# Performance work log

Hardware: AMD Instinct MI355X
Metric: run time of the kernel (lower is better)

## Reference

```python
import jax, jax.numpy as jnp
import numpy as np

N_BLADES = 8  # Cl(3,0): 1, e1, e2, e3 and their products (bitmask blade indexing)


def _blade_sign(a: int, b: int) -> int:
    # Sign from reordering basis vectors when multiplying blades a*b (Euclidean metric).
    a >>= 1
    s = 0
    while a:
        s += bin(a & b).count('1')
        a >>= 1
    return -1 if (s & 1) else 1


def make_cayley() -> np.ndarray:
    C = np.zeros((N_BLADES, N_BLADES, N_BLADES), dtype=np.float32)
    for a in range(N_BLADES):
        for b in range(N_BLADES):
            C[a, b, a ^ b] = float(_blade_sign(a, b))
    return C


def setup_inputs() -> dict:
    key = jax.random.key(0)
    k1, k2 = jax.random.split(key)
    B, Cin, Cout = 8192, 256, 256
    scale = 1.0 / np.sqrt(Cin * N_BLADES)
    x = jax.random.normal(k1, (B, Cin, N_BLADES), dtype=jnp.float32)
    weight = jax.random.normal(k2, (Cout, Cin, N_BLADES), dtype=jnp.float32) * scale
    bias = jnp.zeros((Cout, N_BLADES), dtype=jnp.float32)
    cayley = jnp.asarray(make_cayley())
    return {"x": x, "weight": weight, "bias": bias, "cayley": cayley}


def reference(x, weight, bias, cayley):
    # A[b,o,j,k] = sum_i W[o,i,j] * X[b,i,k]  (weight blade j times input blade k)
    A = jnp.einsum('oij,bik->bojk', weight, x)
    # Contract blade pair (j,k) into output blade l via sparse Cayley table.
    out = jnp.einsum('jkl,bojk->bol', cayley, A)
    return out + bias[None, :, :]
```

## Files before the change

kernel.cpp:

```cpp
#include <hip/hip_runtime.h>
#include <stdint.h>
#include <stddef.h>


typedef __bf16 bf16x8 __attribute__((ext_vector_type(8)));
typedef float  f32x4  __attribute__((ext_vector_type(4)));

#define BM 128
#define BN 128
#define BK 32

__device__ __forceinline__ void async_copy16(void* lds_dst, const void* g_src) {
    __builtin_amdgcn_global_load_lds(
        (__attribute__((address_space(1))) void*)g_src,
        (__attribute__((address_space(3))) void*)lds_dst,
        16, 0, 0);
}

__global__ __launch_bounds__(256) void cast_bf16_kernel(
    const float* __restrict__ in, __bf16* __restrict__ out, long n)
{
    long i = ((long)blockIdx.x * 256 + threadIdx.x) * 8;
    if (i + 8 <= n) {
        const f32x4* p = (const f32x4*)(in + i);
        f32x4 v0 = p[0];
        f32x4 v1 = p[1];
        bf16x8 o;
        o[0] = (__bf16)v0[0]; o[1] = (__bf16)v0[1];
        o[2] = (__bf16)v0[2]; o[3] = (__bf16)v0[3];
        o[4] = (__bf16)v1[0]; o[5] = (__bf16)v1[1];
        o[6] = (__bf16)v1[2]; o[7] = (__bf16)v1[3];
        *(bf16x8*)(out + i) = o;
    }
}

__global__ __launch_bounds__(256) void build_wt_kernel(
    const float* __restrict__ W,
    const float* __restrict__ cayley,
    __bf16* __restrict__ Wt,
    int Cin, int Cout)
{
    __shared__ float Cay[512];
    for (int t = threadIdx.x; t < 512; t += 256) Cay[t] = cayley[t];
    __syncthreads();

    int flat = blockIdx.x * 256 + threadIdx.x;
    int total = Cout * 8 * Cin;
    if (flat >= total) return;
    int i = flat % Cin;
    int n = flat / Cin;
    int o = n >> 3, l = n & 7;

    const float* wrow = W + ((size_t)o * Cin + i) * 8;
    float w8[8];
    #pragma unroll
    for (int j = 0; j < 8; ++j) w8[j] = wrow[j];

    bf16x8 outv;
    #pragma unroll
    for (int k = 0; k < 8; ++k) {
        float s = 0.f;
        #pragma unroll
        for (int j = 0; j < 8; ++j) s += Cay[j * 64 + k * 8 + l] * w8[j];
        outv[k] = (__bf16)s;
    }
    *(bf16x8*)(Wt + (size_t)n * (Cin * 8) + i * 8) = outv;
}

__global__ __launch_bounds__(256) void gemm_bt_kernel(
    const __bf16* __restrict__ A,
    const __bf16* __restrict__ Bt,
    const float*  __restrict__ bias,
    float* __restrict__ C,
    int M, int N, int K)
{
    __shared__ __align__(16) __bf16 As0[BM * BK];
    __shared__ __align__(16) __bf16 As1[BM * BK];
    __shared__ __align__(16) __bf16 Bs0[BN * BK];
    __shared__ __align__(16) __bf16 Bs1[BN * BK];

    const int tid  = threadIdx.x;
    const int wave = tid >> 6;
    const int lane = tid & 63;
    const int quad = lane >> 4;
    const int l16  = lane & 15;

    const int bid   = blockIdx.x;
    const int band  = (bid & 7) | ((bid >> 7) << 3);
    const int ncol  = (bid >> 3) & 15;
    const int mBase = band * BM;
    const int nBase = ncol * BN;

    const int srow = lane >> 2;
    const int sgrp = (lane & 3) ^ ((srow >> 1) & 3);

    const __bf16* gA0 = A  + (size_t)(mBase + (2 * wave + 0) * 16 + srow) * K + sgrp * 8;
    const __bf16* gA1 = A  + (size_t)(mBase + (2 * wave + 1) * 16 + srow) * K + sgrp * 8;
    const __bf16* gB0 = Bt + (size_t)(nBase + (2 * wave + 0) * 16 + srow) * K + sgrp * 8;
    const __bf16* gB1 = Bt + (size_t)(nBase + (2 * wave + 1) * 16 + srow) * K + sgrp * 8;
    const int cOff0 = (2 * wave + 0) * 512;
    const int cOff1 = (2 * wave + 1) * 512;

    const int wm = (wave >> 1) * 64;
    const int wn = (wave & 1) * 64;
    const int offq = (quad ^ ((l16 >> 1) & 3)) * 8;
    const int rowA = (wm + l16) * BK;
    const int rowB = (wn + l16) * BK;

    f32x4 acc[4][4] = {};

#define PREFETCH(BUFA, BUFB, KOFF)                       \
    do {                                                 \
        async_copy16(&BUFA[cOff0], gA0 + (KOFF));        \
        async_copy16(&BUFA[cOff1], gA1 + (KOFF));        \
        async_copy16(&BUFB[cOff0], gB0 + (KOFF));        \
        async_copy16(&BUFB[cOff1], gB1 + (KOFF));        \
    } while (0)

#define COMPUTE(BUFA, BUFB)                                               \
    do {                                                                  \
        const __bf16* fA = &BUFA[rowA] + offq;                            \
        const __bf16* fB = &BUFB[rowB] + offq;                            \
        bf16x8 af[4], bfr[4];                                             \
        _Pragma("unroll")                                                 \
        for (int mt = 0; mt < 4; ++mt)                                    \
            af[mt] = *(const bf16x8*)(fA + mt * 16 * BK);                 \
        _Pragma("unroll")                                                 \
        for (int nt = 0; nt < 4; ++nt)                                    \
            bfr[nt] = *(const bf16x8*)(fB + nt * 16 * BK);                \
        _Pragma("unroll")                                                 \
        for (int mt = 0; mt < 4; ++mt)                                    \
            _Pragma("unroll")                                             \
            for (int nt = 0; nt < 4; ++nt)                                \
                acc[mt][nt] = __builtin_amdgcn_mfma_f32_16x16x32_bf16(    \
                    af[mt], bfr[nt], acc[mt][nt], 0, 0, 0);               \
    } while (0)

    PREFETCH(As0, Bs0, 0);

    int k0 = 0;
    for (; k0 < K - 2 * BK; k0 += 2 * BK) {
        __syncthreads();
        PREFETCH(As1, Bs1, k0 + BK);
        COMPUTE(As0, Bs0);

        __syncthreads();
        PREFETCH(As0, Bs0, k0 + 2 * BK);
        COMPUTE(As1, Bs1);
    }

    __syncthreads();
    PREFETCH(As1, Bs1, k0 + BK);
    COMPUTE(As0, Bs0);

    __syncthreads();
    COMPUTE(As1, Bs1);

#undef PREFETCH
#undef COMPUTE

    float bv[4];
    #pragma unroll
    for (int nt = 0; nt < 4; ++nt)
        bv[nt] = bias[nBase + wn + nt * 16 + l16];

    #pragma unroll
    for (int mt = 0; mt < 4; ++mt) {
        #pragma unroll
        for (int nt = 0; nt < 4; ++nt) {
            const int col = nBase + wn + nt * 16 + l16;
            #pragma unroll
            for (int r = 0; r < 4; ++r) {
                const int row = mBase + wm + mt * 16 + quad * 4 + r;
                C[(size_t)row * N + col] = acc[mt][nt][r] + bv[nt];
            }
        }
    }
}

extern "C" void kernel_launch(void* const* d_in, const int* in_sizes, int n_in,
                              void* d_out, int out_size, void* d_ws, size_t ws_size,
                              hipStream_t stream) {
    const float* x      = (const float*)d_in[0];
    const float* weight = (const float*)d_in[1];
    const float* bias   = (const float*)d_in[2];
    const float* cayley = (const float*)d_in[3];
    float* out = (float*)d_out;

    const int Cout = in_sizes[2] / 8;
    const int Cin  = in_sizes[1] / (Cout * 8);
    const int Bm   = in_sizes[0] / (Cin * 8);
    const int M = Bm;
    const int N = Cout * 8;
    const int K = Cin * 8;

    __bf16* Xb = (__bf16*)d_ws;
    __bf16* Wt = (__bf16*)((char*)d_ws + (size_t)M * K * 2);

    long nx = (long)M * K;
    int castBlocks = (int)(nx / 8 / 256);
    cast_bf16_kernel<<<castBlocks, 256, 0, stream>>>(x, Xb, nx);

    int totalWt = N * Cin;
    build_wt_kernel<<<(totalWt + 255) / 256, 256, 0, stream>>>(weight, cayley, Wt, Cin, Cout);

    int grid = (M / BM) * (N / BN);
    gemm_bt_kernel<<<grid, 256, 0, stream>>>(Xb, Wt, bias, out, M, N, K);
}
```

Baseline: 199.5 us.

## Switch GEMM to 32x32x16 MFMA tiles and merge prep kernels into one launch

The GEMM inner loop moves from sixteen 16x16x32 bf16 MFMAs per wave per K-step to eight 32x32x16 MFMAs over 2x2 accumulator tiles. This cuts the number of LDS fragment loads per MFMA and uses the larger matrix instruction. The epilogue is rewritten to match the 32x32 output layout. Separately, the bf16 cast of x and the Cayley weight fold are merged into a single launch to save one kernel launch, at the cost of branch divergence by block index.

```diff
diff --git a/kernel.cpp b/kernel.cpp
--- a/kernel.cpp
+++ b/kernel.cpp
@@ -3,8 +3,9 @@
 #include <stddef.h>
 
 
-typedef __bf16 bf16x8 __attribute__((ext_vector_type(8)));
-typedef float  f32x4  __attribute__((ext_vector_type(4)));
+typedef __bf16 bf16x8  __attribute__((ext_vector_type(8)));
+typedef float  f32x4   __attribute__((ext_vector_type(4)));
+typedef float  f32x16  __attribute__((ext_vector_type(16)));
 
 #define BM 128
 #define BN 128
@@ -17,34 +18,31 @@
         16, 0, 0);
 }
 
-__global__ __launch_bounds__(256) void cast_bf16_kernel(
-    const float* __restrict__ in, __bf16* __restrict__ out, long n)
-{
-    long i = ((long)blockIdx.x * 256 + threadIdx.x) * 8;
-    if (i + 8 <= n) {
-        const f32x4* p = (const f32x4*)(in + i);
-        f32x4 v0 = p[0];
-        f32x4 v1 = p[1];
-        bf16x8 o;
-        o[0] = (__bf16)v0[0]; o[1] = (__bf16)v0[1];
-        o[2] = (__bf16)v0[2]; o[3] = (__bf16)v0[3];
-        o[4] = (__bf16)v1[0]; o[5] = (__bf16)v1[1];
-        o[6] = (__bf16)v1[2]; o[7] = (__bf16)v1[3];
-        *(bf16x8*)(out + i) = o;
-    }
-}
-
-__global__ __launch_bounds__(256) void build_wt_kernel(
-    const float* __restrict__ W,
-    const float* __restrict__ cayley,
-    __bf16* __restrict__ Wt,
-    int Cin, int Cout)
+__global__ __launch_bounds__(256) void prep_kernel(
+    const float* __restrict__ x, __bf16* __restrict__ Xb, long nx,
+    const float* __restrict__ W, const float* __restrict__ cayley,
+    __bf16* __restrict__ Wt, int Cin, int Cout, int castBlocks)
 {
     __shared__ float Cay[512];
+    if ((int)blockIdx.x < castBlocks) {
+        long i = ((long)blockIdx.x * 256 + threadIdx.x) * 8;
+        if (i + 8 <= nx) {
+            const f32x4* p = (const f32x4*)(x + i);
+            f32x4 v0 = p[0];
+            f32x4 v1 = p[1];
+            bf16x8 o;
+            o[0] = (__bf16)v0[0]; o[1] = (__bf16)v0[1];
+            o[2] = (__bf16)v0[2]; o[3] = (__bf16)v0[3];
+            o[4] = (__bf16)v1[0]; o[5] = (__bf16)v1[1];
+            o[6] = (__bf16)v1[2]; o[7] = (__bf16)v1[3];
+            *(bf16x8*)(Xb + i) = o;
+        }
+        return;
+    }
     for (int t = threadIdx.x; t < 512; t += 256) Cay[t] = cayley[t];
     __syncthreads();
 
-    int flat = blockIdx.x * 256 + threadIdx.x;
+    int flat = (blockIdx.x - castBlocks) * 256 + threadIdx.x;
     int total = Cout * 8 * Cin;
     if (flat >= total) return;
     int i = flat % Cin;
@@ -82,8 +80,8 @@
     const int tid  = threadIdx.x;
     const int wave = tid >> 6;
     const int lane = tid & 63;
-    const int quad = lane >> 4;
-    const int l16  = lane & 15;
+    const int l32  = lane & 31;
+    const int half = lane >> 5;
 
     const int bid   = blockIdx.x;
     const int band  = (bid & 7) | ((bid >> 7) << 3);
@@ -103,11 +101,13 @@
 
     const int wm = (wave >> 1) * 64;
     const int wn = (wave & 1) * 64;
-    const int offq = (quad ^ ((l16 >> 1) & 3)) * 8;
-    const int rowA = (wm + l16) * BK;
-    const int rowB = (wn + l16) * BK;
-
-    f32x4 acc[4][4] = {};
+    const int key = (l32 >> 1) & 3;
+    const int g0  = ((0 + half) ^ key) * 8;
+    const int g1  = ((2 + half) ^ key) * 8;
+    const int rA  = (wm + l32) * BK;
+    const int rB  = (wn + l32) * BK;
+
+    f32x16 acc[2][2] = {};
 
 #define PREFETCH(BUFA, BUFB, KOFF)                       \
     do {                                                 \
@@ -117,23 +117,24 @@
         async_copy16(&BUFB[cOff1], gB1 + (KOFF));        \
     } while (0)
 
-#define COMPUTE(BUFA, BUFB)                                               \
-    do {                                                                  \
-        const __bf16* fA = &BUFA[rowA] + offq;                            \
-        const __bf16* fB = &BUFB[rowB] + offq;                            \
-        bf16x8 af[4], bfr[4];                                             \
-        _Pragma("unroll")                                                 \
-        for (int mt = 0; mt < 4; ++mt)                                    \
-            af[mt] = *(const bf16x8*)(fA + mt * 16 * BK);                 \
-        _Pragma("unroll")                                                 \
-        for (int nt = 0; nt < 4; ++nt)                                    \
-            bfr[nt] = *(const bf16x8*)(fB + nt * 16 * BK);                \
-        _Pragma("unroll")                                                 \
-        for (int mt = 0; mt < 4; ++mt)                                    \
-            _Pragma("unroll")                                             \
-            for (int nt = 0; nt < 4; ++nt)                                \
-                acc[mt][nt] = __builtin_amdgcn_mfma_f32_16x16x32_bf16(    \
-                    af[mt], bfr[nt], acc[mt][nt], 0, 0, 0);               \
+#define COMPUTE(BUFA, BUFB)                                                \
+    do {                                                                   \
+        bf16x8 a00 = *(const bf16x8*)(&BUFA[rA] + g0);                     \
+        bf16x8 a10 = *(const bf16x8*)(&BUFA[rA + 32 * BK] + g0);           \
+        bf16x8 b00 = *(const bf16x8*)(&BUFB[rB] + g0);                     \
+        bf16x8 b10 = *(const bf16x8*)(&BUFB[rB + 32 * BK] + g0);           \
+        bf16x8 a01 = *(const bf16x8*)(&BUFA[rA] + g1);                     \
+        bf16x8 a11 = *(const bf16x8*)(&BUFA[rA + 32 * BK] + g1);           \
+        bf16x8 b01 = *(const bf16x8*)(&BUFB[rB] + g1);                     \
+        bf16x8 b11 = *(const bf16x8*)(&BUFB[rB + 32 * BK] + g1);           \
+        acc[0][0] = __builtin_amdgcn_mfma_f32_32x32x16_bf16(a00, b00, acc[0][0], 0, 0, 0); \
+        acc[0][1] = __builtin_amdgcn_mfma_f32_32x32x16_bf16(a00, b10, acc[0][1], 0, 0, 0); \
+        acc[1][0] = __builtin_amdgcn_mfma_f32_32x32x16_bf16(a10, b00, acc[1][0], 0, 0, 0); \
+        acc[1][1] = __builtin_amdgcn_mfma_f32_32x32x16_bf16(a10, b10, acc[1][1], 0, 0, 0); \
+        acc[0][0] = __builtin_amdgcn_mfma_f32_32x32x16_bf16(a01, b01, acc[0][0], 0, 0, 0); \
+        acc[0][1] = __builtin_amdgcn_mfma_f32_32x32x16_bf16(a01, b11, acc[0][1], 0, 0, 0); \
+        acc[1][0] = __builtin_amdgcn_mfma_f32_32x32x16_bf16(a11, b01, acc[1][0], 0, 0, 0); \
+        acc[1][1] = __builtin_amdgcn_mfma_f32_32x32x16_bf16(a11, b11, acc[1][1], 0, 0, 0); \
     } while (0)
 
     PREFETCH(As0, Bs0, 0);
@@ -159,20 +160,17 @@
 #undef PREFETCH
 #undef COMPUTE
 
-    float bv[4];
     #pragma unroll
-    for (int nt = 0; nt < 4; ++nt)
-        bv[nt] = bias[nBase + wn + nt * 16 + l16];
-
-    #pragma unroll
-    for (int mt = 0; mt < 4; ++mt) {
+    for (int nt = 0; nt < 2; ++nt) {
+        const int col = nBase + wn + nt * 32 + l32;
+        const float bv = bias[col];
         #pragma unroll
-        for (int nt = 0; nt < 4; ++nt) {
-            const int col = nBase + wn + nt * 16 + l16;
+        for (int mt = 0; mt < 2; ++mt) {
+            const int rowBase = mBase + wm + mt * 32 + 4 * half;
             #pragma unroll
-            for (int r = 0; r < 4; ++r) {
-                const int row = mBase + wm + mt * 16 + quad * 4 + r;
-                C[(size_t)row * N + col] = acc[mt][nt][r] + bv[nt];
+            for (int r = 0; r < 16; ++r) {
+                const int row = rowBase + (r & 3) + 8 * (r >> 2);
+                C[(size_t)row * N + col] = acc[mt][nt][r] + bv;
             }
         }
     }
@@ -199,10 +197,9 @@
 
     long nx = (long)M * K;
     int castBlocks = (int)(nx / 8 / 256);
-    cast_bf16_kernel<<<castBlocks, 256, 0, stream>>>(x, Xb, nx);
-
-    int totalWt = N * Cin;
-    build_wt_kernel<<<(totalWt + 255) / 256, 256, 0, stream>>>(weight, cayley, Wt, Cin, Cout);
+    int foldBlocks = (N * Cin + 255) / 256;
+    prep_kernel<<<castBlocks + foldBlocks, 256, 0, stream>>>(
+        x, Xb, nx, weight, cayley, Wt, Cin, Cout, castBlocks);
 
     int grid = (M / BM) * (N / BN);
     gemm_bt_kernel<<<grid, 256, 0, stream>>>(Xb, Wt, bias, out, M, N, K);
```

Result: no change. 202.2 us (+1.4%).
